# Kernel tuning notes

Measured on AMD Instinct MI355X. Metric: run time of the kernel, lower is better.

Reference implementation:

```python
import jax, jax.numpy as jnp
import numpy as np

NUM_HEADS = 16

def setup_inputs() -> dict:
    key = jax.random.key(0)
    ks = jax.random.split(key, 5)
    B, T, C = 2, 2048, 1024
    s = 0.02
    return {
        "x": jax.random.normal(ks[0], (B, T, C), dtype=jnp.float32),
        "attn_w": jax.random.normal(ks[1], (3 * C, C), dtype=jnp.float32) * s,
        "attn_b": jax.random.normal(ks[2], (3 * C,), dtype=jnp.float32) * s,
        "proj_w": jax.random.normal(ks[3], (C, C), dtype=jnp.float32) * s,
        "proj_b": jax.random.normal(ks[4], (C,), dtype=jnp.float32) * s,
    }

def reference(x, attn_w, attn_b, proj_w, proj_b):
    B, T, C = x.shape
    H = NUM_HEADS
    D = C // H
    # fused QKV projection (torch Linear: x @ W^T + b)
    qkv = x @ attn_w.T + attn_b                      # [B, T, 3C]
    q, k, v = jnp.split(qkv, 3, axis=-1)             # each [B, T, C]
    # split heads -> [B, H, T, D]
    def heads(t):
        return t.reshape(B, T, H, D).transpose(0, 2, 1, 3)
    q, k, v = heads(q), heads(k), heads(v)
    scale = 1.0 / jnp.sqrt(jnp.asarray(D, dtype=x.dtype))
    scores = jnp.einsum("bhtd,bhsd->bhts", q, k) * scale   # [B, H, T, T]
    causal = jnp.tril(jnp.ones((T, T), dtype=bool))
    scores = jnp.where(causal[None, None], scores, jnp.asarray(-jnp.inf, dtype=scores.dtype))
    att = jax.nn.softmax(scores, axis=-1)
    out = jnp.einsum("bhts,bhsd->bhtd", att, v)      # [B, H, T, D]
    out = out.transpose(0, 2, 1, 3).reshape(B, T, C)
    return out @ proj_w.T + proj_b
```

## Files before the change

### kernel.cpp

```cpp
#include <hip/hip_runtime.h>
#include <hip/hip_bf16.h>

typedef __bf16 bf16_t;
typedef __bf16 bf16x4 __attribute__((ext_vector_type(4)));
typedef __bf16 bf16x8 __attribute__((ext_vector_type(8)));
typedef float f32x4 __attribute__((ext_vector_type(4)));
typedef float f32x8 __attribute__((ext_vector_type(8)));

#define MFMA16(a, b, c) __builtin_amdgcn_mfma_f32_16x16x32_bf16(a, b, c, 0, 0, 0)

#define GLOAD_LDS16(g, l)                                              \
  __builtin_amdgcn_global_load_lds(                                    \
      (const __attribute__((address_space(1))) unsigned int*)(g),      \
      (__attribute__((address_space(3))) unsigned int*)(l), 16, 0, 0)

constexpr int B = 2, T = 2048, C = 1024, H = 16, D = 64;
constexpr int NQKV = 3 * C;
constexpr int M = B * T;

#define QSCALE 0.18033688011112042f

__global__ __launch_bounds__(256) void cvt_kernel(
    const float* __restrict__ s0, bf16_t* __restrict__ d0, int n0,
    const float* __restrict__ s1, bf16_t* __restrict__ d1, int n1,
    const float* __restrict__ s2, bf16_t* __restrict__ d2, int n2)
{
  const float* s; bf16_t* d; int n;
  if (blockIdx.y == 0)      { s = s0; d = d0; n = n0; }
  else if (blockIdx.y == 1) { s = s1; d = d1; n = n1; }
  else                      { s = s2; d = d2; n = n2; }
  const int idx = (blockIdx.x * 256 + threadIdx.x) * 8;
  if (idx >= n) return;
  f32x8 t = *(const f32x8*)(s + idx);
  bf16x8 r;
#pragma unroll
  for (int j = 0; j < 8; ++j) r[j] = (bf16_t)t[j];
  *(bf16x8*)(d + idx) = r;
}

template<int BM, int BN, int MI, int NI>
__device__ __forceinline__ void gemm_mainloop_db(
    const bf16_t* __restrict__ A, const bf16_t* __restrict__ Wt,
    const int K, const int m0, const int n0,
    bf16_t* ldsA0, bf16_t* ldsA1, bf16_t* ldsB0, bf16_t* ldsB1,
    f32x4 acc[MI][NI])
{
  const int tid  = threadIdx.x;
  const int wv   = tid >> 6;
  const int lane = tid & 63;
  const int col  = lane & 15;
  const int quad = lane >> 4;
  const int lr8  = lane >> 3;
  const int cpos = lane & 7;
  const int wm = wv >> 1, wn = wv & 1;
  constexpr int AJ = BM / 32;
  constexpr int ARW = BM / 4;
  constexpr int BJ = BN / 32;
  constexpr int BRW = BN / 4;

  const bf16_t* ag[AJ]; const bf16_t* bg[BJ];
#pragma unroll
  for (int j = 0; j < AJ; ++j)
    ag[j] = A + (size_t)(m0 + wv * ARW + j * 8 + lr8) * K + (cpos ^ lr8) * 8;
#pragma unroll
  for (int j = 0; j < BJ; ++j)
    bg[j] = Wt + (size_t)(n0 + wv * BRW + j * 8 + lr8) * K + (cpos ^ lr8) * 8;

  const int xa = quad ^ (col & 7);
  const int niter = K / 64;

#pragma unroll
  for (int j = 0; j < AJ; ++j)
    GLOAD_LDS16(ag[j], ldsA0 + (wv * ARW + j * 8) * 64);
#pragma unroll
  for (int j = 0; j < BJ; ++j)
    GLOAD_LDS16(bg[j], ldsB0 + (wv * BRW + j * 8) * 64);

  for (int it = 0; it < niter; ++it) {
    __syncthreads();
    const bf16_t* cA = (it & 1) ? ldsA1 : ldsA0;
    const bf16_t* cB = (it & 1) ? ldsB1 : ldsB0;
    if (it + 1 < niter) {
      bf16_t* nA = (it & 1) ? ldsA0 : ldsA1;
      bf16_t* nB = (it & 1) ? ldsB0 : ldsB1;
      const int off = (it + 1) * 64;
#pragma unroll
      for (int j = 0; j < AJ; ++j)
        GLOAD_LDS16(ag[j] + off, nA + (wv * ARW + j * 8) * 64);
#pragma unroll
      for (int j = 0; j < BJ; ++j)
        GLOAD_LDS16(bg[j] + off, nB + (wv * BRW + j * 8) * 64);
    }
#pragma unroll
    for (int ks = 0; ks < 2; ++ks) {
      const int xk = (xa ^ (ks * 4)) * 8;
      bf16x8 af[MI], bfr[NI];
#pragma unroll
      for (int mi = 0; mi < MI; ++mi)
        af[mi] = *(const bf16x8*)(cA + (wm * (MI * 16) + mi * 16 + col) * 64 + xk);
#pragma unroll
      for (int ni = 0; ni < NI; ++ni)
        bfr[ni] = *(const bf16x8*)(cB + (wn * (NI * 16) + ni * 16 + col) * 64 + xk);
#pragma unroll
      for (int mi = 0; mi < MI; ++mi)
#pragma unroll
        for (int ni = 0; ni < NI; ++ni)
          acc[mi][ni] = MFMA16(af[mi], bfr[ni], acc[mi][ni]);
    }
  }
}

__global__ __launch_bounds__(256) void qkv_gemm_kernel(
    const bf16_t* __restrict__ x, const bf16_t* __restrict__ w,
    const float* __restrict__ bias,
    bf16_t* __restrict__ qws, bf16_t* __restrict__ kws, bf16_t* __restrict__ vws)
{
  __shared__ __align__(16) bf16_t ldsA[2][128 * 64];
  __shared__ __align__(16) bf16_t ldsB[2][64 * 64];
  const int lane = threadIdx.x & 63;
  const int wv   = threadIdx.x >> 6;
  const int col  = lane & 15;
  const int quad = lane >> 4;
  const int wm = wv >> 1, wn = wv & 1;
  const int m0 = blockIdx.y * 128;
  const int n0 = blockIdx.x * 64;

  f32x4 acc[4][2] = {};
  gemm_mainloop_db<128, 64, 4, 2>(x, w, C, m0, n0,
                                  ldsA[0], ldsA[1], ldsB[0], ldsB[1], acc);

  const int which = n0 >> 10;

  if (which == 2) {
    __syncthreads();
    bf16_t* vt = &ldsA[0][0] + wv * 2048;

#pragma unroll
    for (int ni = 0; ni < 2; ++ni) {
      const int n = n0 + wn * 32 + ni * 16 + col;
      const float bval = bias[n];
      const int dl = ni * 16 + col;
#pragma unroll
      for (int r = 0; r < 4; ++r) {
        bf16x4 pw;
#pragma unroll
        for (int mi = 0; mi < 4; ++mi)
          pw[mi] = (bf16_t)(acc[mi][ni][r] + bval);
        const int k = 2 * quad + (r >> 1);
        const int S = dl * 8 + (k ^ (dl & 7));
        *(bf16x4*)(vt + S * 8 + (r & 1) * 4) = pw;
      }
    }

    const int b   = (m0 + wm * 64) >> 11;
    const int t0w = (m0 + wm * 64) & (T - 1);
    const int h   = (n0 & (C - 1)) >> 6;
    const size_t bh = (size_t)(b * H + h);
    const int lr8 = lane >> 3;
    const int c8  = lane & 7;
#pragma unroll
    for (int j = 0; j < 4; ++j) {
      const int dl = j * 8 + lr8;
      const int d  = wn * 32 + dl;
      bf16x8 row = *(const bf16x8*)(vt + (dl * 8 + (c8 ^ (dl & 7))) * 8);
      *(bf16x8*)(vws + (bh * D + d) * T + t0w + c8 * 8) = row;
    }
  } else {
#pragma unroll
    for (int ni = 0; ni < 2; ++ni) {
      const int n = n0 + wn * 32 + ni * 16 + col;
      const float bval = bias[n];
      const int c = n & (C - 1);
      const int h = c >> 6;
      const int d = c & 63;
#pragma unroll
      for (int mi = 0; mi < 4; ++mi) {
#pragma unroll
        for (int r = 0; r < 4; ++r) {
          const int m = m0 + wm * 64 + mi * 16 + quad * 4 + r;
          const int b = m >> 11;
          const int t = m & (T - 1);
          const size_t bh = (size_t)(b * H + h);
          if (which == 0)
            qws[(bh * T + t) * D + d] = (bf16_t)((acc[mi][ni][r] + bval) * QSCALE);
          else
            kws[(bh * T + t) * D + d] = (bf16_t)(acc[mi][ni][r] + bval);
        }
      }
    }
  }
}

__global__ __launch_bounds__(256) void attn_kernel(
    const bf16_t* __restrict__ qws, const bf16_t* __restrict__ kws,
    const bf16_t* __restrict__ vws, bf16_t* __restrict__ yws)
{
  const int id = blockIdx.x;
  const int bh = id & 31;
  const int pr = id >> 5;
  const int tid  = threadIdx.x;
  const int wv   = tid >> 6;
  const int lane = tid & 63;
  const int col  = lane & 15;
  const int quad = lane >> 4;

  const bf16_t* Q  = qws + (size_t)bh * T * D;
  const bf16_t* K  = kws + (size_t)bh * T * D;
  const bf16_t* Vt = vws + (size_t)bh * D * T;

  __shared__ __align__(16) bf16_t ldsK[2][64 * 64];
  __shared__ __align__(16) bf16_t ldsV[2][64 * 64];
  __shared__ __align__(16) bf16_t ldsP[4][16 * 64];
  bf16_t* ldsPw = ldsP[wv];

  const int xs   = col & 7;
  const int cxq  = (quad ^ xs) * 8;
  const int lr8  = lane >> 3;
  const int ksrc = (lane & 7) ^ lr8;
  const int pxor = (quad & 1) * 4;
  const int b = bh >> 4;
  const int h = bh & 15;

  const int qt_h = 31 - pr, qt_l = pr;
  const int t0h = qt_h * 64, t0l = qt_l * 64;
  const int twh = t0h + 16 * wv, twl = t0l + 16 * wv;
  const int niter = qt_h + 1;

  bf16x8 qfh0 = *(const bf16x8*)(Q + (size_t)(twh + col) * D + quad * 8);
  bf16x8 qfh1 = *(const bf16x8*)(Q + (size_t)(twh + col) * D + 32 + quad * 8);
  bf16x8 qfl0 = *(const bf16x8*)(Q + (size_t)(twl + col) * D + quad * 8);
  bf16x8 qfl1 = *(const bf16x8*)(Q + (size_t)(twl + col) * D + 32 + quad * 8);

  f32x4 oh[4] = {}, ol[4] = {};
  f32x4 lph = {}, lpl = {};

  auto compute_tile = [&](const bf16_t* bK, const bf16_t* bV, int s0, int tw,
                          int t0, bf16x8 qf0, bf16x8 qf1,
                          f32x4 (&o)[4], f32x4& lp) {
    f32x4 sc[4];
#pragma unroll
    for (int kb = 0; kb < 4; ++kb) {
      const bf16_t* kr = bK + (kb * 16 + col) * 64;
      bf16x8 kf0 = *(const bf16x8*)(kr + cxq);
      bf16x8 kf1 = *(const bf16x8*)(kr + (cxq ^ 32));
      f32x4 a = {};
      a = MFMA16(qf0, kf0, a);
      a = MFMA16(qf1, kf1, a);
      sc[kb] = a;
    }
    if (s0 == t0) {
#pragma unroll
      for (int r = 0; r < 4; ++r) {
        const int prow = (quad * 4 + r) * 64;
        const int pxr  = pxor + r;
        bf16x4 pw;
#pragma unroll
        for (int kb = 0; kb < 4; ++kb) {
          float p = __builtin_amdgcn_exp2f(sc[kb][r]);
          if (s0 + kb * 16 + col > tw + quad * 4 + r) p = 0.0f;
          lp[r] += p;
          pw[kb] = (bf16_t)p;
        }
        *(bf16x4*)(ldsPw + prow + (((col >> 1) ^ pxr) * 8) + (col & 1) * 4) = pw;
      }
    } else {
#pragma unroll
      for (int r = 0; r < 4; ++r) {
        const int prow = (quad * 4 + r) * 64;
        const int pxr  = pxor + r;
        bf16x4 pw;
#pragma unroll
        for (int kb = 0; kb < 4; ++kb) {
          float p = __builtin_amdgcn_exp2f(sc[kb][r]);
          lp[r] += p;
          pw[kb] = (bf16_t)p;
        }
        *(bf16x4*)(ldsPw + prow + (((col >> 1) ^ pxr) * 8) + (col & 1) * 4) = pw;
      }
    }
#pragma unroll
    for (int ks = 0; ks < 2; ++ks) {
      const int xk = cxq ^ (ks * 32);
      bf16x8 pa = *(const bf16x8*)(ldsPw + col * 64 + xk);
#pragma unroll
      for (int ni = 0; ni < 4; ++ni) {
        bf16x8 vf = *(const bf16x8*)(bV + (ni * 16 + col) * 64 + xk);
        o[ni] = MFMA16(pa, vf, o[ni]);
      }
    }
  };

#pragma unroll
  for (int j = 0; j < 2; ++j) {
    GLOAD_LDS16(K + (size_t)(16 * wv + j * 8 + lr8) * D + ksrc * 8,
                ldsK[0] + (16 * wv + j * 8) * 64);
    GLOAD_LDS16(Vt + (size_t)(16 * wv + j * 8 + lr8) * T + ksrc * 8,
                ldsV[0] + (16 * wv + j * 8) * 64);
  }

  for (int it = 0; it < niter; ++it) {
    const int s0 = it * 64;
    __syncthreads();

    if (it + 1 < niter) {
      const int sn = s0 + 64;
      bf16_t* dK = ldsK[(it + 1) & 1];
      bf16_t* dV = ldsV[(it + 1) & 1];
#pragma unroll
      for (int j = 0; j < 2; ++j) {
        GLOAD_LDS16(K + (size_t)(sn + 16 * wv + j * 8 + lr8) * D + ksrc * 8,
                    dK + (16 * wv + j * 8) * 64);
        GLOAD_LDS16(Vt + (size_t)(16 * wv + j * 8 + lr8) * T + sn + ksrc * 8,
                    dV + (16 * wv + j * 8) * 64);
      }
    }

    const bf16_t* bK = ldsK[it & 1];
    const bf16_t* bV = ldsV[it & 1];

    compute_tile(bK, bV, s0, twh, t0h, qfh0, qfh1, oh, lph);
    if (s0 <= t0l)
      compute_tile(bK, bV, s0, twl, t0l, qfl0, qfl1, ol, lpl);
  }

#pragma unroll
  for (int r = 0; r < 4; ++r) {
    float l0 = lph[r], l1 = lpl[r];
#pragma unroll
    for (int off = 1; off < 16; off <<= 1) {
      l0 += __shfl_xor(l0, off);
      l1 += __shfl_xor(l1, off);
    }
    const float rl0 = 1.0f / l0, rl1 = 1.0f / l1;
    const int th = twh + quad * 4 + r;
    const int tl = twl + quad * 4 + r;
#pragma unroll
    for (int ni = 0; ni < 4; ++ni) {
      const int d = ni * 16 + col;
      yws[((size_t)(b * T + th)) * C + h * D + d] = (bf16_t)(oh[ni][r] * rl0);
      yws[((size_t)(b * T + tl)) * C + h * D + d] = (bf16_t)(ol[ni][r] * rl1);
    }
  }
}

__global__ __launch_bounds__(256) void proj_gemm_kernel(
    const bf16_t* __restrict__ y, const bf16_t* __restrict__ w,
    const float* __restrict__ bias, float* __restrict__ out)
{
  __shared__ __align__(16) bf16_t ldsA[2][64 * 64];
  __shared__ __align__(16) bf16_t ldsB[2][64 * 64];
  const int lane = threadIdx.x & 63;
  const int wv   = threadIdx.x >> 6;
  const int col  = lane & 15;
  const int quad = lane >> 4;
  const int wm = wv >> 1, wn = wv & 1;
  const int m0 = blockIdx.y * 64;
  const int n0 = blockIdx.x * 64;

  f32x4 acc[2][2] = {};
  gemm_mainloop_db<64, 64, 2, 2>(y, w, C, m0, n0,
                                 ldsA[0], ldsA[1], ldsB[0], ldsB[1], acc);

#pragma unroll
  for (int ni = 0; ni < 2; ++ni) {
    const int n = n0 + wn * 32 + ni * 16 + col;
    const float bval = bias[n];
#pragma unroll
    for (int mi = 0; mi < 2; ++mi) {
#pragma unroll
      for (int r = 0; r < 4; ++r) {
        const int m = m0 + wm * 32 + mi * 16 + quad * 4 + r;
        out[(size_t)m * C + n] = acc[mi][ni][r] + bval;
      }
    }
  }
}

extern "C" void kernel_launch(void* const* d_in, const int* in_sizes, int n_in,
                              void* d_out, int out_size, void* d_ws, size_t ws_size,
                              hipStream_t stream) {
  const float* x      = (const float*)d_in[0];
  const float* attn_w = (const float*)d_in[1];
  const float* attn_b = (const float*)d_in[2];
  const float* proj_w = (const float*)d_in[3];
  const float* proj_b = (const float*)d_in[4];
  float* out = (float*)d_out;

  const size_t E = (size_t)B * H * T * D;
  char* ws = (char*)d_ws;
  bf16_t* qws = (bf16_t*)(ws);
  bf16_t* kws = (bf16_t*)(ws + 2 * E);
  bf16_t* vws = (bf16_t*)(ws + 4 * E);
  bf16_t* yws = (bf16_t*)(ws + 6 * E);
  bf16_t* xb  = (bf16_t*)(ws + 8 * E);
  bf16_t* awb = (bf16_t*)(ws + 10 * E);
  bf16_t* pwb = (bf16_t*)(ws + 11 * E + E / 2);

  const int NX = M * C, NAW = NQKV * C, NPW = C * C;
  cvt_kernel<<<dim3(NX / 2048, 3), 256, 0, stream>>>(
      x, xb, NX, attn_w, awb, NAW, proj_w, pwb, NPW);
  qkv_gemm_kernel<<<dim3(NQKV / 64, M / 128), 256, 0, stream>>>(
      xb, awb, attn_b, qws, kws, vws);
  attn_kernel<<<512, 256, 0, stream>>>(qws, kws, vws, yws);
  proj_gemm_kernel<<<dim3(C / 64, M / 64), 256, 0, stream>>>(
      yws, pwb, proj_b, out);
}
```

Before: 170.6 us.

## Split causal attention loop into phases, separate P buffers, add MFMA priority hints

Splits the key-tile loop into four phases (both query tiles active, low-tile diagonal, high tile only, high-tile diagonal), so the diagonal mask check and the per-iteration branch on whether the low tile is active are gone from the steady-state loop. Each query tile now gets its own per-wave P buffer in LDS, so the two tiles' softmax writes and PV reads no longer go through one shared scratch area and can be interleaved more freely. It also wraps the MFMA sections in s_setprio hints so waves doing matrix work get issue priority. The cost is more LDS per block, which may lower occupancy, and larger code from the repeated tile bodies.

```diff
diff --git a/kernel.cpp b/kernel.cpp
--- a/kernel.cpp
+++ b/kernel.cpp
@@ -210,8 +210,10 @@
 
   __shared__ __align__(16) bf16_t ldsK[2][64 * 64];
   __shared__ __align__(16) bf16_t ldsV[2][64 * 64];
-  __shared__ __align__(16) bf16_t ldsP[4][16 * 64];
-  bf16_t* ldsPw = ldsP[wv];
+  __shared__ __align__(16) bf16_t ldsPh_s[4][16 * 64];
+  __shared__ __align__(16) bf16_t ldsPl_s[4][16 * 64];
+  bf16_t* ldsPh = ldsPh_s[wv];
+  bf16_t* ldsPl = ldsPl_s[wv];
 
   const int xs   = col & 7;
   const int cxq  = (quad ^ xs) * 8;
@@ -224,7 +226,6 @@
   const int qt_h = 31 - pr, qt_l = pr;
   const int t0h = qt_h * 64, t0l = qt_l * 64;
   const int twh = t0h + 16 * wv, twl = t0l + 16 * wv;
-  const int niter = qt_h + 1;
 
   bf16x8 qfh0 = *(const bf16x8*)(Q + (size_t)(twh + col) * D + quad * 8);
   bf16x8 qfh1 = *(const bf16x8*)(Q + (size_t)(twh + col) * D + 32 + quad * 8);
@@ -234,10 +235,24 @@
   f32x4 oh[4] = {}, ol[4] = {};
   f32x4 lph = {}, lpl = {};
 
+  auto stage = [&](int it) {
+    const int sn = it * 64;
+    bf16_t* dK = ldsK[it & 1];
+    bf16_t* dV = ldsV[it & 1];
+#pragma unroll
+    for (int j = 0; j < 2; ++j) {
+      GLOAD_LDS16(K + (size_t)(sn + 16 * wv + j * 8 + lr8) * D + ksrc * 8,
+                  dK + (16 * wv + j * 8) * 64);
+      GLOAD_LDS16(Vt + (size_t)(16 * wv + j * 8 + lr8) * T + sn + ksrc * 8,
+                  dV + (16 * wv + j * 8) * 64);
+    }
+  };
+
   auto compute_tile = [&](const bf16_t* bK, const bf16_t* bV, int s0, int tw,
-                          int t0, bf16x8 qf0, bf16x8 qf1,
-                          f32x4 (&o)[4], f32x4& lp) {
+                          bf16x8 qf0, bf16x8 qf1,
+                          f32x4 (&o)[4], f32x4& lp, bf16_t* Pw, bool diag) {
     f32x4 sc[4];
+    __builtin_amdgcn_s_setprio(1);
 #pragma unroll
     for (int kb = 0; kb < 4; ++kb) {
       const bf16_t* kr = bK + (kb * 16 + col) * 64;
@@ -248,79 +263,67 @@
       a = MFMA16(qf1, kf1, a);
       sc[kb] = a;
     }
-    if (s0 == t0) {
-#pragma unroll
-      for (int r = 0; r < 4; ++r) {
-        const int prow = (quad * 4 + r) * 64;
-        const int pxr  = pxor + r;
-        bf16x4 pw;
-#pragma unroll
-        for (int kb = 0; kb < 4; ++kb) {
-          float p = __builtin_amdgcn_exp2f(sc[kb][r]);
-          if (s0 + kb * 16 + col > tw + quad * 4 + r) p = 0.0f;
-          lp[r] += p;
-          pw[kb] = (bf16_t)p;
-        }
-        *(bf16x4*)(ldsPw + prow + (((col >> 1) ^ pxr) * 8) + (col & 1) * 4) = pw;
+    __builtin_amdgcn_s_setprio(0);
+#pragma unroll
+    for (int r = 0; r < 4; ++r) {
+      const int prow = (quad * 4 + r) * 64;
+      const int pxr  = pxor + r;
+      bf16x4 pw;
+#pragma unroll
+      for (int kb = 0; kb < 4; ++kb) {
+        float p = __builtin_amdgcn_exp2f(sc[kb][r]);
+        if (diag && (s0 + kb * 16 + col > tw + quad * 4 + r)) p = 0.0f;
+        lp[r] += p;
+        pw[kb] = (bf16_t)p;
       }
-    } else {
-#pragma unroll
-      for (int r = 0; r < 4; ++r) {
-        const int prow = (quad * 4 + r) * 64;
-        const int pxr  = pxor + r;
-        bf16x4 pw;
-#pragma unroll
-        for (int kb = 0; kb < 4; ++kb) {
-          float p = __builtin_amdgcn_exp2f(sc[kb][r]);
-          lp[r] += p;
-          pw[kb] = (bf16_t)p;
-        }
-        *(bf16x4*)(ldsPw + prow + (((col >> 1) ^ pxr) * 8) + (col & 1) * 4) = pw;
-      }
-    }
+      *(bf16x4*)(Pw + prow + (((col >> 1) ^ pxr) * 8) + (col & 1) * 4) = pw;
+    }
+    __builtin_amdgcn_s_setprio(1);
 #pragma unroll
     for (int ks = 0; ks < 2; ++ks) {
       const int xk = cxq ^ (ks * 32);
-      bf16x8 pa = *(const bf16x8*)(ldsPw + col * 64 + xk);
+      bf16x8 pa = *(const bf16x8*)(Pw + col * 64 + xk);
 #pragma unroll
       for (int ni = 0; ni < 4; ++ni) {
         bf16x8 vf = *(const bf16x8*)(bV + (ni * 16 + col) * 64 + xk);
         o[ni] = MFMA16(pa, vf, o[ni]);
       }
     }
+    __builtin_amdgcn_s_setprio(0);
   };
 
-#pragma unroll
-  for (int j = 0; j < 2; ++j) {
-    GLOAD_LDS16(K + (size_t)(16 * wv + j * 8 + lr8) * D + ksrc * 8,
-                ldsK[0] + (16 * wv + j * 8) * 64);
-    GLOAD_LDS16(Vt + (size_t)(16 * wv + j * 8 + lr8) * T + ksrc * 8,
-                ldsV[0] + (16 * wv + j * 8) * 64);
-  }
-
-  for (int it = 0; it < niter; ++it) {
-    const int s0 = it * 64;
-    __syncthreads();
-
-    if (it + 1 < niter) {
-      const int sn = s0 + 64;
-      bf16_t* dK = ldsK[(it + 1) & 1];
-      bf16_t* dV = ldsV[(it + 1) & 1];
-#pragma unroll
-      for (int j = 0; j < 2; ++j) {
-        GLOAD_LDS16(K + (size_t)(sn + 16 * wv + j * 8 + lr8) * D + ksrc * 8,
-                    dK + (16 * wv + j * 8) * 64);
-        GLOAD_LDS16(Vt + (size_t)(16 * wv + j * 8 + lr8) * T + sn + ksrc * 8,
-                    dV + (16 * wv + j * 8) * 64);
-      }
-    }
-
+  stage(0);
+
+  for (int it = 0; it < qt_l; ++it) {
+    __syncthreads();
+    stage(it + 1);
     const bf16_t* bK = ldsK[it & 1];
     const bf16_t* bV = ldsV[it & 1];
-
-    compute_tile(bK, bV, s0, twh, t0h, qfh0, qfh1, oh, lph);
-    if (s0 <= t0l)
-      compute_tile(bK, bV, s0, twl, t0l, qfl0, qfl1, ol, lpl);
+    compute_tile(bK, bV, it * 64, twh, qfh0, qfh1, oh, lph, ldsPh, false);
+    compute_tile(bK, bV, it * 64, twl, qfl0, qfl1, ol, lpl, ldsPl, false);
+  }
+  {
+    const int it = qt_l;
+    __syncthreads();
+    stage(it + 1);
+    const bf16_t* bK = ldsK[it & 1];
+    const bf16_t* bV = ldsV[it & 1];
+    compute_tile(bK, bV, it * 64, twh, qfh0, qfh1, oh, lph, ldsPh, false);
+    compute_tile(bK, bV, it * 64, twl, qfl0, qfl1, ol, lpl, ldsPl, true);
+  }
+  for (int it = qt_l + 1; it < qt_h; ++it) {
+    __syncthreads();
+    stage(it + 1);
+    const bf16_t* bK = ldsK[it & 1];
+    const bf16_t* bV = ldsV[it & 1];
+    compute_tile(bK, bV, it * 64, twh, qfh0, qfh1, oh, lph, ldsPh, false);
+  }
+  {
+    const int it = qt_h;
+    __syncthreads();
+    const bf16_t* bK = ldsK[it & 1];
+    const bf16_t* bV = ldsV[it & 1];
+    compute_tile(bK, bV, it * 64, twh, qfh0, qfh1, oh, lph, ldsPh, true);
   }
 
 #pragma unroll
```

New measurement: 170.2 us. No clear change (-0.2%).
